# Performance work log

Hardware: AMD Instinct MI355X
Metric: run time of the kernel (lower is better)

Reference implementation:

```python
import jax, jax.numpy as jnp
import numpy as np

B = 2; L = 64; HOP = 256; T = L * HOP
IN_CH = 101; INNER = 128; COND = 81
NBLOCK = 2; LAYERS = 5; K = 3; KH = 64
COUT = 2 * INNER
KCH = INNER * COUT * K * LAYERS   # 491520
BCH = COUT * LAYERS               # 1280


def setup_inputs() -> dict:
    key = jax.random.key(0)
    ks = jax.random.split(key, 12)
    n = lambda k, s, sc: jax.random.normal(k, s, jnp.float32) * sc
    return {
        "x": n(ks[0], (B, IN_CH, T), 1.0),
        "c": n(ks[1], (B, COND, L), 1.0),
        "fc_W": n(ks[2], (INNER, IN_CH), 0.1),
        "fc_b": jnp.zeros((INNER,), jnp.float32),
        "inp_W": n(ks[3], (NBLOCK, KH, COND, 5), 0.05),
        "inp_b": jnp.zeros((NBLOCK, KH), jnp.float32),
        "res1_W": n(ks[4], (NBLOCK, KH, KH), 0.1),
        "res1_b": jnp.zeros((NBLOCK, KH), jnp.float32),
        "res2_W": n(ks[5], (NBLOCK, KH, KH), 0.1),
        "res2_b": jnp.zeros((NBLOCK, KH), jnp.float32),
        "kern_W": n(ks[6], (NBLOCK, KCH, KH), 0.02),
        "kern_b": jnp.zeros((NBLOCK, KCH), jnp.float32),
        "biasc_W": n(ks[7], (NBLOCK, BCH, KH), 0.02),
        "biasc_b": jnp.zeros((NBLOCK, BCH), jnp.float32),
        "lc1_W": n(ks[8], (INNER, INNER), 0.08),
        "lc1_b": jnp.zeros((INNER,), jnp.float32),
        "lc2_W": n(ks[9], (1, INNER), 0.08),
        "lc2_b": jnp.zeros((1,), jnp.float32),
    }


def _conv1x1(x, W, b):
    return jnp.einsum('oc,bcl->bol', W, x) + b[None, :, None]


def _conv5(x, W, b):
    y = jax.lax.conv_general_dilated(x, W, (1,), [(2, 2)],
                                     dimension_numbers=('NCH', 'OIH', 'NCH'))
    return y + b[None, :, None]


def _lrelu(x):
    return jnp.where(x >= 0, x, 0.1 * x)


def _kernel_predictor(c, iW, ib, r1W, r1b, r2W, r2b, kW, kb, bW, bb):
    h = _lrelu(_conv5(c, iW, ib))
    h = h + _conv1x1(_lrelu(_conv1x1(h, r1W, r1b)), r2W, r2b)
    k = _conv1x1(h, kW, kb)   # (B, KCH, L)
    bb_ = _conv1x1(h, bW, bb)  # (B, BCH, L)
    Bn, _, Ln = c.shape
    kernels = k.reshape(Bn, LAYERS, INNER, COUT, K, Ln)
    bias = bb_.reshape(Bn, LAYERS, COUT, Ln)
    return kernels, bias


def _lvc(x, kernel, bias, dilation, hop):
    # x: (B, Cin, T); kernel: (B, Cin, Cout, K, L); bias: (B, Cout, L)
    Bn, Cin, Tn = x.shape
    _, _, O, Kn, Ln = kernel.shape
    p = dilation * (Kn - 1) // 2
    xp = jnp.pad(x, ((0, 0), (0, 0), (p, p)))
    win = hop + 2 * p
    # per-window gather (unfold over time with stride hop)
    idx = (jnp.arange(Ln) * hop)[:, None] + jnp.arange(win)[None, :]
    xw = xp[:, :, idx]
    m = win // dilation                                  # hop/d + (K-1)
    xt = xw.reshape(Bn, Cin, Ln, m, dilation).transpose(0, 1, 2, 4, 3)  # (B,Cin,L,d,m)
    S = hop // dilation
    idx2 = jnp.arange(S)[:, None] + jnp.arange(Kn)[None, :]  # (S, K) sliding taps
    xu = xt[..., idx2]                                   # (B, Cin, L, d, S, K)
    o = jnp.einsum('bildsk,biokl->bolsd', xu, kernel)
    o = o + bias[:, :, :, None, None]
    return o.reshape(Bn, O, Tn)


def _lvc_block(x, c, iW, ib, r1W, r1b, r2W, r2b, kW, kb, bW, bb):
    kernels, bias = _kernel_predictor(c, iW, ib, r1W, r1b, r2W, r2b, kW, kb, bW, bb)
    for i in range(LAYERS):
        d = 2 ** i  # max 16 < hop, so hop<dilation branch never triggers
        y = _lvc(x, kernels[:, i], bias[:, i], d, HOP)
        x = jax.nn.sigmoid(y[:, :INNER]) * jnp.tanh(y[:, INNER:])
    return x


def reference(x, c, fc_W, fc_b, inp_W, inp_b, res1_W, res1_b, res2_W, res2_b,
              kern_W, kern_b, biasc_W, biasc_b, lc1_W, lc1_b, lc2_W, lc2_b):
    h = _conv1x1(x, fc_W, fc_b)
    for n_ in range(NBLOCK):
        y = _lvc_block(h, c, inp_W[n_], inp_b[n_], res1_W[n_], res1_b[n_],
                       res2_W[n_], res2_b[n_], kern_W[n_], kern_b[n_],
                       biasc_W[n_], biasc_b[n_])
        h = y if n_ == 0 else h + y
    h = jnp.maximum(h, 0.0)
    h = _conv1x1(h, lc1_W, lc1_b)
    h = jnp.maximum(h, 0.0)
    h = _conv1x1(h, lc2_W, lc2_b)
    return h
```

## Files before the change

### kernel.cpp

```cpp
#include <hip/hip_runtime.h>
#include <math.h>

#define BB     2
#define LSEG   64
#define HOP    256
#define TT     (LSEG*HOP)
#define IN_CH  101
#define INNER  128
#define COND   81
#define LAYERS 5
#define KTAP   3
#define KH     64
#define COUT   256
#define RPL    (INNER*COUT*KTAP)
#define KCH    (RPL*LAYERS)
#define BCH    (COUT*LAYERS)
#define NBL    (BB*LSEG)
#define XS     36

typedef _Float16 f16;
typedef _Float16 f16x2 __attribute__((ext_vector_type(2)));
typedef _Float16 f16x4 __attribute__((ext_vector_type(4)));
typedef _Float16 f16x8 __attribute__((ext_vector_type(8)));
typedef float    f32x4 __attribute__((ext_vector_type(4)));

__global__ __launch_bounds__(256) void k_fc(const float* __restrict__ x,
                                            const float* __restrict__ W,
                                            const float* __restrict__ bias,
                                            f16* __restrict__ out) {
    int half = blockIdx.x & 1;
    int g = (blockIdx.x >> 1)*256 + threadIdx.x;
    int b = g / TT, t = g % TT;
    float xv[IN_CH];
    const float* xp = x + (size_t)b*IN_CH*TT + t;
#pragma unroll
    for (int c = 0; c < IN_CH; ++c) xv[c] = xp[(size_t)c*TT];
    f16* op = out + (size_t)b*INNER*TT + t;
    int o0 = half*64;
    for (int o = o0; o < o0 + 64; ++o) {
        const float* wr = W + o*IN_CH;
        float a0 = bias[o], a1 = 0.f, a2 = 0.f, a3 = 0.f;
#pragma unroll
        for (int c = 0; c + 3 < IN_CH; c += 4) {
            a0 += wr[c]*xv[c]; a1 += wr[c+1]*xv[c+1];
            a2 += wr[c+2]*xv[c+2]; a3 += wr[c+3]*xv[c+3];
        }
        a0 += wr[100]*xv[100];
        op[(size_t)o*TT] = (f16)((a0+a1)+(a2+a3));
    }
}

__global__ __launch_bounds__(256) void k_h1(const float* __restrict__ cc,
                                            const float* __restrict__ iW,
                                            const float* __restrict__ ib,
                                            float* __restrict__ h1buf) {
    int og = blockIdx.x & 7;
    int bp = blockIdx.x >> 3;
    int b  = bp & 1;
    int n  = bp >> 1;
    __shared__ float cL[COND*LSEG];
    __shared__ float wL[8*COND*5];
    int tid = threadIdx.x;
    for (int idx = tid; idx < COND*LSEG; idx += 256)
        cL[idx] = cc[(size_t)b*COND*LSEG + idx];
    const float* wsrc = iW + (size_t)n*KH*COND*5 + (size_t)og*8*COND*5;
    for (int idx = tid; idx < 8*COND*5; idx += 256)
        wL[idx] = wsrc[idx];
    __syncthreads();
#pragma unroll
    for (int rep = 0; rep < 2; ++rep) {
        int idx = rep*256 + tid;
        int ol = idx >> 6, l = idx & 63;
        int o  = og*8 + ol;
        float acc = ib[n*KH + o];
        const float* wrow = wL + ol*COND*5;
        for (int i = 0; i < COND; ++i) {
            const float* crow = cL + i*LSEG;
            const float* w5 = wrow + i*5;
#pragma unroll
            for (int k = 0; k < 5; ++k) {
                int ll = l + k - 2;
                if (ll >= 0 && ll < LSEG) acc += crow[ll]*w5[k];
            }
        }
        h1buf[(((size_t)(n*BB + b))*KH + o)*LSEG + l] = acc >= 0.f ? acc : 0.1f*acc;
    }
}

__global__ __launch_bounds__(256) void k_h2t(const float* __restrict__ h1buf,
                                             const float* __restrict__ r1W,
                                             const float* __restrict__ r1b,
                                             const float* __restrict__ r2W,
                                             const float* __restrict__ r2b,
                                             float* __restrict__ h2buf,
                                             f16* __restrict__ h2h) {
    int b = blockIdx.x & 1;
    int n = blockIdx.x >> 1;
    __shared__ float h1L[KH*LSEG];
    __shared__ float t1L[KH*LSEG];
    __shared__ float wL[KH*KH];
    int tid = threadIdx.x;
    const float* h1src = h1buf + ((size_t)(n*BB + b))*KH*LSEG;
    for (int idx = tid; idx < KH*LSEG; idx += 256)
        h1L[idx] = h1src[idx];
    for (int idx = tid; idx < KH*KH; idx += 256)
        wL[idx] = r1W[(size_t)n*KH*KH + idx];
    __syncthreads();
#pragma unroll
    for (int rep = 0; rep < 16; ++rep) {
        int idx = rep*256 + tid;
        int o = idx >> 6, l = idx & 63;
        float acc = r1b[n*KH + o];
        const float* wr = wL + o*KH;
#pragma unroll
        for (int i = 0; i < KH; ++i) acc += wr[i]*h1L[i*LSEG + l];
        t1L[idx] = acc >= 0.f ? acc : 0.1f*acc;
    }
    __syncthreads();
    for (int idx = tid; idx < KH*KH; idx += 256)
        wL[idx] = r2W[(size_t)n*KH*KH + idx];
    __syncthreads();
#pragma unroll
    for (int rep = 0; rep < 16; ++rep) {
        int idx = rep*256 + tid;
        int o = idx >> 6, l = idx & 63;
        float acc = r2b[n*KH + o];
        const float* wr = wL + o*KH;
#pragma unroll
        for (int i = 0; i < KH; ++i) acc += wr[i]*t1L[i*LSEG + l];
        float h2 = h1L[o*LSEG + l] + acc;
        size_t row = (size_t)n*NBL + b*LSEG + l;
        h2buf[row*KH + o] = h2;
        h2h  [row*KH + o] = (f16)h2;
    }
}

__global__ __launch_bounds__(256) void k_biash(const float* __restrict__ bW,
                                               const float* __restrict__ bb,
                                               const float* __restrict__ h2buf,
                                               float* __restrict__ biasbuf) {
    int tg = blockIdx.x*256 + threadIdx.x;
    int n  = __builtin_amdgcn_readfirstlane(tg / (BB*BCH));
    int rem = tg - n*(BB*BCH);
    int b  = __builtin_amdgcn_readfirstlane(rem / BCH);
    int rb = rem % BCH;
    float w[KH];
    const float4* wp = (const float4*)(bW + ((size_t)n*BCH + rb)*KH);
#pragma unroll
    for (int q = 0; q < KH/4; ++q) {
        float4 v = wp[q];
        w[4*q] = v.x; w[4*q+1] = v.y; w[4*q+2] = v.z; w[4*q+3] = v.w;
    }
    float bv = bb[n*BCH + rb];
    for (int l = 0; l < LSEG; ++l) {
        size_t row = (size_t)n*NBL + b*LSEG + l;
        const float* h2 = h2buf + row*KH;
        float a0 = bv, a1 = 0.f, a2 = 0.f, a3 = 0.f;
#pragma unroll
        for (int j = 0; j < KH; j += 4) {
            a0 += w[j]*h2[j]; a1 += w[j+1]*h2[j+1];
            a2 += w[j+2]*h2[j+2]; a3 += w[j+3]*h2[j+3];
        }
        biasbuf[row*BCH + rb] = (a0+a1)+(a2+a3);
    }
}

__global__ __launch_bounds__(256) void k_gen(const float* __restrict__ kW,
                                             const float* __restrict__ kb,
                                             const f16*   __restrict__ h2h,
                                             f16*         __restrict__ kbuf) {
    int o   = blockIdx.x & 255;
    int tmp = blockIdx.x >> 8;
    int tap = tmp % 3;  tmp /= 3;
    int lay = tmp % 5;
    int n   = tmp / 5;
    int lane = threadIdx.x & 63;
    int wm   = threadIdx.x >> 6;
    int n16  = lane & 15;
    int quad = lane >> 4;

    size_t rbase = (size_t)n*KCH + (size_t)lay*RPL;
    const f16* h2b = h2h + (size_t)n*NBL*KH;

    f16x8 afr[2][2];
#pragma unroll
    for (int j = 0; j < 2; ++j) {
        int c = wm*32 + j*16 + n16;
        const float* arow = kW + (rbase + (size_t)(c*COUT + o)*KTAP + tap)*KH;
#pragma unroll
        for (int ks = 0; ks < 2; ++ks) {
            float4 v0 = *(const float4*)(arow + ks*32 + quad*8);
            float4 v1 = *(const float4*)(arow + ks*32 + quad*8 + 4);
            afr[j][ks] = f16x8{(f16)v0.x,(f16)v0.y,(f16)v0.z,(f16)v0.w,
                               (f16)v1.x,(f16)v1.y,(f16)v1.z,(f16)v1.w};
        }
    }
    f32x4 bini[2];
#pragma unroll
    for (int j = 0; j < 2; ++j) {
#pragma unroll
        for (int r = 0; r < 4; ++r) {
            int c = wm*32 + j*16 + quad*4 + r;
            bini[j][r] = kb[rbase + (size_t)(c*COUT + o)*KTAP + tap];
        }
    }
    int op = (o < 128) ? 2*o : 2*(o-128) + 1;
    size_t obase = (size_t)op*384 + (size_t)tap*128;
    f16* kout = kbuf + ((size_t)(n*LAYERS + lay)*NBL)*RPL + obase;

#pragma unroll 2
    for (int t = 0; t < 8; ++t) {
        int bl = t*16 + n16;
        const f16* brow = h2b + (size_t)bl*KH;
        f16x8 bf0 = *(const f16x8*)(brow + quad*8);
        f16x8 bf1 = *(const f16x8*)(brow + 32 + quad*8);
        f32x4 acc0 = bini[0], acc1 = bini[1];
        acc0 = __builtin_amdgcn_mfma_f32_16x16x32_f16(afr[0][0], bf0, acc0, 0, 0, 0);
        acc0 = __builtin_amdgcn_mfma_f32_16x16x32_f16(afr[0][1], bf1, acc0, 0, 0, 0);
        acc1 = __builtin_amdgcn_mfma_f32_16x16x32_f16(afr[1][0], bf0, acc1, 0, 0, 0);
        acc1 = __builtin_amdgcn_mfma_f32_16x16x32_f16(afr[1][1], bf1, acc1, 0, 0, 0);
        int c0 = wm*32 + quad*4;
        *(f16x4*)(kout + (size_t)bl*RPL + c0) =
            f16x4{(f16)acc0[0],(f16)acc0[1],(f16)acc0[2],(f16)acc0[3]};
        *(f16x4*)(kout + (size_t)bl*RPL + c0 + 16) =
            f16x4{(f16)acc1[0],(f16)acc1[1],(f16)acc1[2],(f16)acc1[3]};
    }
}

template<int DIL>
__global__ __launch_bounds__(256) void k_lvc(const f16* __restrict__ xin,
                                             const f16* __restrict__ kbuf,
                                             const float* __restrict__ biasbuf,
                                             f16* __restrict__ xout,
                                             int layerIdx) {
    constexpr int WIN = 128 + 2*DIL;
    int wg  = blockIdx.x;
    int o0  = (wg & 3)*64;
    int th  = (wg >> 2) & 1;
    int l   = (wg >> 3) & 63;
    int b   = wg >> 9;
    int bl  = b*LSEG + l;
    int tid = threadIdx.x;
    int w   = tid >> 6;
    int lane = tid & 63;
    int quad = lane >> 4;
    int n16  = lane & 15;
    int wo = (w & 1)*32;
    int wt = (w >> 1)*64;

    __shared__ f16 As[3*64*XS];
    __shared__ f16 xwin[WIN*XS];

    const float* bias_l = biasbuf + (size_t)bl*BCH + layerIdx*COUT;
    f32x4 acc[2][4];
#pragma unroll
    for (int j = 0; j < 2; ++j) {
        int g0 = (o0 + wo + j*16 + quad*4) >> 1;
        f32x4 ini;
        ini[0] = bias_l[g0];       ini[1] = bias_l[g0 + 128];
        ini[2] = bias_l[g0 + 1];   ini[3] = bias_l[g0 + 1 + 128];
#pragma unroll
        for (int tt = 0; tt < 4; ++tt) acc[j][tt] = ini;
    }

    const f16* xb = xin + (size_t)b*INNER*TT;
    const f16* kbl = kbuf + (size_t)bl*RPL + (size_t)o0*384;
    int o_l = tid >> 2, q4 = tid & 3;
    int gt0 = l*256 + th*128 - DIL;

    for (int cb = 0; cb < 4; ++cb) {
        for (int cc = w; cc < 32; cc += 4) {
            const f16* src = xb + (size_t)(cb*32 + cc)*TT;
#pragma unroll
            for (int tw0 = 0; tw0 < WIN; tw0 += 64) {
                int tw = tw0 + lane;
                if (tw < WIN) {
                    int gt = gt0 + tw;
                    f16 v = ((unsigned)gt < (unsigned)TT) ? src[gt] : (f16)0.f;
                    xwin[tw*XS + cc] = v;
                }
            }
        }
#pragma unroll
        for (int tap = 0; tap < 3; ++tap) {
            f16x8 v = *(const f16x8*)&kbl[(size_t)o_l*384 + tap*128 + cb*32 + q4*8];
            *(f16x8*)&As[(tap*64 + o_l)*XS + q4*8] = v;
        }
        __syncthreads();
#pragma unroll
        for (int tap = 0; tap < 3; ++tap) {
            f16x8 af0 = *(const f16x8*)&As[(tap*64 + wo + n16)*XS + quad*8];
            f16x8 af1 = *(const f16x8*)&As[(tap*64 + wo + 16 + n16)*XS + quad*8];
#pragma unroll
            for (int tt = 0; tt < 4; ++tt) {
                int trow = wt + tt*16 + n16 + tap*DIL;
                f16x8 bf = *(const f16x8*)&xwin[trow*XS + quad*8];
                acc[0][tt] = __builtin_amdgcn_mfma_f32_16x16x32_f16(af0, bf, acc[0][tt], 0, 0, 0);
                acc[1][tt] = __builtin_amdgcn_mfma_f32_16x16x32_f16(af1, bf, acc[1][tt], 0, 0, 0);
            }
        }
        __syncthreads();
    }
    f16* ob = xout + (size_t)b*INNER*TT + l*256 + th*128;
#pragma unroll
    for (int j = 0; j < 2; ++j) {
        int g0 = (o0 + wo + j*16 + quad*4) >> 1;
#pragma unroll
        for (int tt = 0; tt < 4; ++tt) {
            int tloc = wt + tt*16 + n16;
            f32x4 a = acc[j][tt];
            float s0  = 1.f/(1.f + __expf(-a[0]));
            float th0 = 2.f/(1.f + __expf(-2.f*a[1])) - 1.f;
            float s1  = 1.f/(1.f + __expf(-a[2]));
            float th1 = 2.f/(1.f + __expf(-2.f*a[3])) - 1.f;
            ob[(size_t)g0*TT + tloc]     = (f16)(s0*th0);
            ob[(size_t)(g0+1)*TT + tloc] = (f16)(s1*th1);
        }
    }
}

__global__ __launch_bounds__(256) void k_head(const f16* __restrict__ y0,
                                              const f16* __restrict__ y1,
                                              const float* __restrict__ W1,
                                              const float* __restrict__ b1,
                                              const float* __restrict__ W2,
                                              const float* __restrict__ b2,
                                              float* __restrict__ out) {
    int b    = blockIdx.x >> 8;
    int tseg = (blockIdx.x & 255)*64;
    int tid  = threadIdx.x;
    int w    = tid >> 6;
    int lane = tid & 63;
    int t    = tseg + lane;
    __shared__ float red[4][64];

    float h[INNER];
    const f16* p0 = y0 + (size_t)b*INNER*TT + t;
    const f16* p1 = y1 + (size_t)b*INNER*TT + t;
#pragma unroll
    for (int c = 0; c < INNER; ++c) {
        float v = (float)p0[(size_t)c*TT] + (float)p1[(size_t)c*TT];
        h[c] = v > 0.f ? v : 0.f;
    }
    float part = 0.f;
    int oBase = w*32;
    for (int oi = 0; oi < 32; ++oi) {
        int o = oBase + oi;
        const float* wr = W1 + o*INNER;
        float z0 = b1[o], z1 = 0.f, z2 = 0.f, z3 = 0.f;
#pragma unroll
        for (int c = 0; c < INNER; c += 4) {
            z0 += wr[c]*h[c];   z1 += wr[c+1]*h[c+1];
            z2 += wr[c+2]*h[c+2]; z3 += wr[c+3]*h[c+3];
        }
        float z = (z0+z1)+(z2+z3);
        z = z > 0.f ? z : 0.f;
        part += W2[o]*z;
    }
    red[w][lane] = part;
    __syncthreads();
    if (w == 0) {
        float acc = b2[0] + red[0][lane] + red[1][lane] + red[2][lane] + red[3][lane];
        out[(size_t)b*TT + t] = acc;
    }
}

extern "C" void kernel_launch(void* const* d_in, const int* in_sizes, int n_in,
                              void* d_out, int out_size, void* d_ws, size_t ws_size,
                              hipStream_t stream) {
    const float* x    = (const float*)d_in[0];
    const float* c    = (const float*)d_in[1];
    const float* fcW  = (const float*)d_in[2];
    const float* fcb  = (const float*)d_in[3];
    const float* inpW = (const float*)d_in[4];
    const float* inpb = (const float*)d_in[5];
    const float* r1W  = (const float*)d_in[6];
    const float* r1b  = (const float*)d_in[7];
    const float* r2W  = (const float*)d_in[8];
    const float* r2b  = (const float*)d_in[9];
    const float* kW   = (const float*)d_in[10];
    const float* kb   = (const float*)d_in[11];
    const float* bW   = (const float*)d_in[12];
    const float* bb   = (const float*)d_in[13];
    const float* l1W  = (const float*)d_in[14];
    const float* l1b  = (const float*)d_in[15];
    const float* l2W  = (const float*)d_in[16];
    const float* l2b  = (const float*)d_in[17];

    float* ws = (float*)d_ws;
    float* h2buf   = ws;
    float* biasbuf = h2buf + (size_t)2*NBL*KH;
    float* h1buf   = biasbuf + (size_t)2*NBL*BCH;
    f16*   h2h     = (f16*)(h1buf + (size_t)2*BB*KH*LSEG);
    f16*   bufA    = h2h + (size_t)2*NBL*KH;
    f16*   bufB    = bufA + (size_t)BB*INNER*TT;
    f16*   bufC    = bufB + (size_t)BB*INNER*TT;
    f16*   kbuf    = bufC + (size_t)BB*INNER*TT;

    k_fc<<<BB*TT/256*2, 256, 0, stream>>>(x, fcW, fcb, bufA);

    k_h1<<<32, 256, 0, stream>>>(c, inpW, inpb, h1buf);
    k_h2t<<<4, 256, 0, stream>>>(h1buf, r1W, r1b, r2W, r2b, h2buf, h2h);
    k_biash<<<20, 256, 0, stream>>>(bW, bb, h2buf, biasbuf);
    k_gen<<<2*LAYERS*3*256, 256, 0, stream>>>(kW, kb, h2h, kbuf);

    for (int n = 0; n < 2; ++n) {
        const float* bias_n = biasbuf + (size_t)n*NBL*BCH;
        f16* pin = (n == 0) ? bufA : bufB;
        f16* s0  = (n == 0) ? bufB : bufC;
        f16* s1  = (n == 0) ? bufC : bufA;
        f16* cin = pin;
        for (int i = 0; i < LAYERS; ++i) {
            const f16* kslice = kbuf + (size_t)(n*LAYERS + i)*NBL*RPL;
            f16* cout_ = (i % 2 == 0) ? s0 : s1;
            switch (i) {
                case 0: k_lvc<1> <<<BB*LSEG*2*4, 256, 0, stream>>>(cin, kslice, bias_n, cout_, i); break;
                case 1: k_lvc<2> <<<BB*LSEG*2*4, 256, 0, stream>>>(cin, kslice, bias_n, cout_, i); break;
                case 2: k_lvc<4> <<<BB*LSEG*2*4, 256, 0, stream>>>(cin, kslice, bias_n, cout_, i); break;
                case 3: k_lvc<8> <<<BB*LSEG*2*4, 256, 0, stream>>>(cin, kslice, bias_n, cout_, i); break;
                case 4: k_lvc<16><<<BB*LSEG*2*4, 256, 0, stream>>>(cin, kslice, bias_n, cout_, i); break;
            }
            cin = cout_;
        }
    }
    k_head<<<BB*TT/64, 256, 0, stream>>>(bufB, bufC, l1W, l1b, l2W, l2b, (float*)d_out);
}
```

Measured before the change: 1.139 ms.

## Stage k_gen weights and outputs through LDS; merge k_lvc time halves into 512-thread blocks

k_gen now loads each weight slice with coalesced float4 reads into shared memory, converts it to f16 there, and stages the MFMA results in LDS before writing them out as contiguous 16-byte stores. The old code used strided per-lane global loads and scattered 8-byte stores. k_lvc now has one 512-thread workgroup cover a full 256-sample hop instead of two 128-sample halves, so the kernel slice is loaded once per segment and the dilation halo is read once. The larger workgroup halves the grid (512 blocks) and uses more LDS per block, which may lower occupancy.

```diff
diff --git a/kernel.cpp b/kernel.cpp
--- a/kernel.cpp
+++ b/kernel.cpp
@@ -17,6 +17,8 @@
 #define BCH    (COUT*LAYERS)
 #define NBL    (BB*LSEG)
 #define XS     36
+#define AS_STR 72
+#define CS_STR 136
 
 typedef _Float16 f16;
 typedef _Float16 f16x2 __attribute__((ext_vector_type(2)));
@@ -174,39 +176,43 @@
     int tap = tmp % 3;  tmp /= 3;
     int lay = tmp % 5;
     int n   = tmp / 5;
-    int lane = threadIdx.x & 63;
-    int wm   = threadIdx.x >> 6;
+    int tid  = threadIdx.x;
+    int lane = tid & 63;
+    int wm   = tid >> 6;
     int n16  = lane & 15;
     int quad = lane >> 4;
 
+    __shared__ f16 smem[128*CS_STR];
+    __shared__ float biasL[128];
+
     size_t rbase = (size_t)n*KCH + (size_t)lay*RPL;
     const f16* h2b = h2h + (size_t)n*NBL*KH;
 
+#pragma unroll
+    for (int it = 0; it < 8; ++it) {
+        int g = it*256 + tid;
+        int c = g >> 4, f4i = g & 15;
+        const float4* arow = (const float4*)(kW + (rbase + (size_t)(c*COUT + o)*KTAP + tap)*KH);
+        float4 v = arow[f4i];
+        *(f16x4*)&smem[c*AS_STR + f4i*4] = f16x4{(f16)v.x,(f16)v.y,(f16)v.z,(f16)v.w};
+    }
+    if (tid < 128)
+        biasL[tid] = kb[rbase + (size_t)(tid*COUT + o)*KTAP + tap];
+    __syncthreads();
+
     f16x8 afr[2][2];
+    f32x4 bini[2];
 #pragma unroll
     for (int j = 0; j < 2; ++j) {
         int c = wm*32 + j*16 + n16;
-        const float* arow = kW + (rbase + (size_t)(c*COUT + o)*KTAP + tap)*KH;
-#pragma unroll
-        for (int ks = 0; ks < 2; ++ks) {
-            float4 v0 = *(const float4*)(arow + ks*32 + quad*8);
-            float4 v1 = *(const float4*)(arow + ks*32 + quad*8 + 4);
-            afr[j][ks] = f16x8{(f16)v0.x,(f16)v0.y,(f16)v0.z,(f16)v0.w,
-                               (f16)v1.x,(f16)v1.y,(f16)v1.z,(f16)v1.w};
-        }
-    }
-    f32x4 bini[2];
-#pragma unroll
-    for (int j = 0; j < 2; ++j) {
-#pragma unroll
-        for (int r = 0; r < 4; ++r) {
-            int c = wm*32 + j*16 + quad*4 + r;
-            bini[j][r] = kb[rbase + (size_t)(c*COUT + o)*KTAP + tap];
-        }
-    }
-    int op = (o < 128) ? 2*o : 2*(o-128) + 1;
-    size_t obase = (size_t)op*384 + (size_t)tap*128;
-    f16* kout = kbuf + ((size_t)(n*LAYERS + lay)*NBL)*RPL + obase;
+#pragma unroll
+        for (int ks = 0; ks < 2; ++ks)
+            afr[j][ks] = *(const f16x8*)&smem[c*AS_STR + ks*32 + quad*8];
+#pragma unroll
+        for (int r = 0; r < 4; ++r)
+            bini[j][r] = biasL[wm*32 + j*16 + quad*4 + r];
+    }
+    __syncthreads();
 
 #pragma unroll 2
     for (int t = 0; t < 8; ++t) {
@@ -220,25 +226,34 @@
         acc1 = __builtin_amdgcn_mfma_f32_16x16x32_f16(afr[1][0], bf0, acc1, 0, 0, 0);
         acc1 = __builtin_amdgcn_mfma_f32_16x16x32_f16(afr[1][1], bf1, acc1, 0, 0, 0);
         int c0 = wm*32 + quad*4;
-        *(f16x4*)(kout + (size_t)bl*RPL + c0) =
+        *(f16x4*)&smem[bl*CS_STR + c0] =
             f16x4{(f16)acc0[0],(f16)acc0[1],(f16)acc0[2],(f16)acc0[3]};
-        *(f16x4*)(kout + (size_t)bl*RPL + c0 + 16) =
+        *(f16x4*)&smem[bl*CS_STR + c0 + 16] =
             f16x4{(f16)acc1[0],(f16)acc1[1],(f16)acc1[2],(f16)acc1[3]};
     }
+    __syncthreads();
+
+    int op = (o < 128) ? 2*o : 2*(o-128) + 1;
+    f16* kout = kbuf + ((size_t)(n*LAYERS + lay)*NBL)*RPL + (size_t)op*384 + (size_t)tap*128;
+#pragma unroll
+    for (int it = 0; it < 8; ++it) {
+        int g = it*256 + tid;
+        int row = g >> 4, seg = g & 15;
+        *(f16x8*)(kout + (size_t)row*RPL + seg*8) = *(const f16x8*)&smem[row*CS_STR + seg*8];
+    }
 }
 
 template<int DIL>
-__global__ __launch_bounds__(256) void k_lvc(const f16* __restrict__ xin,
+__global__ __launch_bounds__(512) void k_lvc(const f16* __restrict__ xin,
                                              const f16* __restrict__ kbuf,
                                              const float* __restrict__ biasbuf,
                                              f16* __restrict__ xout,
                                              int layerIdx) {
-    constexpr int WIN = 128 + 2*DIL;
+    constexpr int WIN = 256 + 2*DIL;
     int wg  = blockIdx.x;
     int o0  = (wg & 3)*64;
-    int th  = (wg >> 2) & 1;
-    int l   = (wg >> 3) & 63;
-    int b   = wg >> 9;
+    int l   = (wg >> 2) & 63;
+    int b   = wg >> 8;
     int bl  = b*LSEG + l;
     int tid = threadIdx.x;
     int w   = tid >> 6;
@@ -249,7 +264,7 @@
     int wt = (w >> 1)*64;
 
     __shared__ f16 As[3*64*XS];
-    __shared__ f16 xwin[WIN*XS];
+    __shared__ f16 xwin[288*XS];
 
     const float* bias_l = biasbuf + (size_t)bl*BCH + layerIdx*COUT;
     f32x4 acc[2][4];
@@ -265,11 +280,11 @@
 
     const f16* xb = xin + (size_t)b*INNER*TT;
     const f16* kbl = kbuf + (size_t)bl*RPL + (size_t)o0*384;
-    int o_l = tid >> 2, q4 = tid & 3;
-    int gt0 = l*256 + th*128 - DIL;
+    int o_l = (tid & 255) >> 2, q4 = tid & 3;
+    int gt0 = l*256 - DIL;
 
     for (int cb = 0; cb < 4; ++cb) {
-        for (int cc = w; cc < 32; cc += 4) {
+        for (int cc = w; cc < 32; cc += 8) {
             const f16* src = xb + (size_t)(cb*32 + cc)*TT;
 #pragma unroll
             for (int tw0 = 0; tw0 < WIN; tw0 += 64) {
@@ -281,10 +296,12 @@
                 }
             }
         }
-#pragma unroll
-        for (int tap = 0; tap < 3; ++tap) {
-            f16x8 v = *(const f16x8*)&kbl[(size_t)o_l*384 + tap*128 + cb*32 + q4*8];
-            *(f16x8*)&As[(tap*64 + o_l)*XS + q4*8] = v;
+        if (tid < 256) {
+#pragma unroll
+            for (int tap = 0; tap < 3; ++tap) {
+                f16x8 v = *(const f16x8*)&kbl[(size_t)o_l*384 + tap*128 + cb*32 + q4*8];
+                *(f16x8*)&As[(tap*64 + o_l)*XS + q4*8] = v;
+            }
         }
         __syncthreads();
 #pragma unroll
@@ -301,7 +318,7 @@
         }
         __syncthreads();
     }
-    f16* ob = xout + (size_t)b*INNER*TT + l*256 + th*128;
+    f16* ob = xout + (size_t)b*INNER*TT + l*256;
 #pragma unroll
     for (int j = 0; j < 2; ++j) {
         int g0 = (o0 + wo + j*16 + quad*4) >> 1;
@@ -414,11 +431,11 @@
             const f16* kslice = kbuf + (size_t)(n*LAYERS + i)*NBL*RPL;
             f16* cout_ = (i % 2 == 0) ? s0 : s1;
             switch (i) {
-                case 0: k_lvc<1> <<<BB*LSEG*2*4, 256, 0, stream>>>(cin, kslice, bias_n, cout_, i); break;
-                case 1: k_lvc<2> <<<BB*LSEG*2*4, 256, 0, stream>>>(cin, kslice, bias_n, cout_, i); break;
-                case 2: k_lvc<4> <<<BB*LSEG*2*4, 256, 0, stream>>>(cin, kslice, bias_n, cout_, i); break;
-                case 3: k_lvc<8> <<<BB*LSEG*2*4, 256, 0, stream>>>(cin, kslice, bias_n, cout_, i); break;
-                case 4: k_lvc<16><<<BB*LSEG*2*4, 256, 0, stream>>>(cin, kslice, bias_n, cout_, i); break;
+                case 0: k_lvc<1> <<<BB*LSEG*4, 512, 0, stream>>>(cin, kslice, bias_n, cout_, i); break;
+                case 1: k_lvc<2> <<<BB*LSEG*4, 512, 0, stream>>>(cin, kslice, bias_n, cout_, i); break;
+                case 2: k_lvc<4> <<<BB*LSEG*4, 512, 0, stream>>>(cin, kslice, bias_n, cout_, i); break;
+                case 3: k_lvc<8> <<<BB*LSEG*4, 512, 0, stream>>>(cin, kslice, bias_n, cout_, i); break;
+                case 4: k_lvc<16><<<BB*LSEG*4, 512, 0, stream>>>(cin, kslice, bias_n, cout_, i); break;
             }
             cin = cout_;
         }
```

Result: faster. 1.009 ms (-11.4%).
